# Optimization experiments

Hardware: AMD Instinct MI355X
Metric: run time of the kernel (lower is better)

The kernel has to match this reference:

```python
import jax, jax.numpy as jnp
import numpy as np

NEG_SLOPE = 0.2


def gat_layer(x_src, x_dst, src, dst, W, a_src, a_dst, b, n_dst, H, C):
    # Linear transform: [Ns, H, C] / [Nd, H, C]
    h_s = (x_src @ W).reshape(-1, H, C)
    h_d = (x_dst @ W).reshape(-1, H, C)
    # Per-edge attention logits: a . [x_i || x_j] (x_i = dst/target, x_j = src)
    e = jnp.einsum('ehc,hc->eh', h_s[src], a_src) + jnp.einsum('ehc,hc->eh', h_d[dst], a_dst)
    e = jax.nn.leaky_relu(e, NEG_SLOPE)  # [E, H]
    # Segment softmax over destination neighborhoods
    m = jax.ops.segment_max(e, dst, num_segments=n_dst)          # [Nd, H]
    ex = jnp.exp(e - m[dst])
    denom = jax.ops.segment_sum(ex, dst, num_segments=n_dst)    # [Nd, H]
    alpha = ex / denom[dst]                                      # [E, H]
    # Weighted scatter-sum aggregation
    out = jax.ops.segment_sum(alpha[:, :, None] * h_s[src], dst, num_segments=n_dst)
    return out.reshape(n_dst, H * C) + b


def setup_inputs() -> dict:
    key = jax.random.key(0)
    ks = jax.random.split(key, 16)
    N, F_IN, OUT = 200000, 602, 41
    N1, N1D, E1 = 120000, 30000, 960000
    N2D, E2 = 6000, 192000
    s = 0.05
    return {
        'x': jax.random.normal(ks[0], (N, F_IN), jnp.float32),
        'n_id1': jax.random.randint(ks[1], (N1,), 0, N),
        'res_n_id1': jax.random.randint(ks[2], (N1D,), 0, N1),
        'edge_src1': jax.random.randint(ks[3], (E1,), 0, N1),
        'edge_dst1': jax.random.randint(ks[4], (E1,), 0, N1D),
        'res_n_id2': jax.random.randint(ks[5], (N2D,), 0, N1D),
        'edge_src2': jax.random.randint(ks[6], (E2,), 0, N1D),
        'edge_dst2': jax.random.randint(ks[7], (E2,), 0, N2D),
        'W1': jax.random.normal(ks[8], (F_IN, 64), jnp.float32) * s,
        'att_src1': jax.random.normal(ks[9], (8, 8), jnp.float32) * s,
        'att_dst1': jax.random.normal(ks[10], (8, 8), jnp.float32) * s,
        'bias1': jax.random.normal(ks[11], (64,), jnp.float32) * s,
        'W2': jax.random.normal(ks[12], (64, OUT), jnp.float32) * s,
        'att_src2': jax.random.normal(ks[13], (1, OUT), jnp.float32) * s,
        'att_dst2': jax.random.normal(ks[14], (1, OUT), jnp.float32) * s,
        'bias2': jax.random.normal(ks[15], (OUT,), jnp.float32) * s,
    }


def reference(x, n_id1, res_n_id1, edge_src1, edge_dst1, res_n_id2, edge_src2,
              edge_dst2, W1, att_src1, att_dst1, bias1, W2, att_src2, att_dst2, bias2):
    # Block 1: gather frontier, GATConv(in -> 8, heads=8, concat) -> [N1D, 64]
    h = x[n_id1]
    h = gat_layer(h, h[res_n_id1], edge_src1, edge_dst1,
                  W1, att_src1, att_dst1, bias1, res_n_id1.shape[0], 8, 8)
    h = jax.nn.elu(h)
    # (dropout p=0.6 is identity in eval mode)
    # Block 2: GATConv(64 -> out, heads=1) -> [N2D, out]
    h = gat_layer(h, h[res_n_id2], edge_src2, edge_dst2,
                  W2, att_src2, att_dst2, bias2, res_n_id2.shape[0], 1, W2.shape[1])
    return jax.nn.log_softmax(h, axis=1)
```

## Files before the change

### kernel.cpp

```cpp
#include <hip/hip_runtime.h>
#include <hip/hip_bf16.h>
#include <math.h>

typedef __attribute__((ext_vector_type(8))) short short8;
typedef __attribute__((ext_vector_type(4))) float float4v;

__device__ __forceinline__ float wave_max64(float v) {
#pragma unroll
  for (int o = 32; o > 0; o >>= 1) v = fmaxf(v, __shfl_xor(v, o));
  return v;
}
__device__ __forceinline__ float wave_sum64(float v) {
#pragma unroll
  for (int o = 32; o > 0; o >>= 1) v += __shfl_xor(v, o);
  return v;
}
__device__ __forceinline__ float lrelu02(float v) { return v > 0.f ? v : 0.2f * v; }
__device__ __forceinline__ short bf16_rne(float f) {
  unsigned u = __builtin_bit_cast(unsigned, f);
  unsigned r = (u + 0x7FFFu + ((u >> 16) & 1u)) >> 16;
  return (short)r;
}

__global__ void hist_prepack_kernel(const int* __restrict__ dst1, const int* __restrict__ dst2,
                                    int* __restrict__ counts, const float* __restrict__ W,
                                    short* __restrict__ Wp, int E1, int E2, int N1D, int nbE) {
  int b = blockIdx.x;
  if (b < nbE) {
    int e = b * 256 + threadIdx.x;
    if (e < E1) atomicAdd(&counts[dst1[e]], 1);
    else if (e < E1 + E2) atomicAdd(&counts[N1D + dst2[e - E1]], 1);
  } else {
    int idx = (b - nbE) * 256 + threadIdx.x;
    if (idx >= 19 * 4 * 64) return;
    int lane = idx & 63;
    int t = (idx >> 6) & 3;
    int s = idx >> 8;
    int quad = lane >> 4, n = t * 16 + (lane & 15);
    short8 v;
#pragma unroll
    for (int j = 0; j < 8; j++) {
      int k = s * 32 + quad * 8 + j;
      v[j] = (k < 602) ? bf16_rne(W[k * 64 + n]) : (short)0;
    }
    *((short8*)Wp + idx) = v;
  }
}

__global__ __launch_bounds__(256) void scan1_kernel(const int* __restrict__ counts,
                                                    int* __restrict__ offs,
                                                    int* __restrict__ bsum, int n) {
  __shared__ int ws[4], wpre[4];
  int tid = threadIdx.x, lane = tid & 63, w = tid >> 6;
  int i = blockIdx.x * 256 + tid;
  int v = (i < n) ? counts[i] : 0;
  int x = v;
#pragma unroll
  for (int o = 1; o < 64; o <<= 1) {
    int y = __shfl_up(x, o);
    if (lane >= o) x += y;
  }
  if (lane == 63) ws[w] = x;
  __syncthreads();
  if (tid == 0) {
    int run = 0;
#pragma unroll
    for (int k = 0; k < 4; k++) { wpre[k] = run; run += ws[k]; }
    bsum[blockIdx.x] = run;
  }
  __syncthreads();
  if (i < n) offs[i] = x - v + wpre[w];
}

__global__ __launch_bounds__(256) void scan2_kernel(int* __restrict__ bsum, int nb) {
  __shared__ int ws[4], wpre[4];
  int tid = threadIdx.x, lane = tid & 63, w = tid >> 6;
  int v = (tid < nb) ? bsum[tid] : 0;
  int x = v;
#pragma unroll
  for (int o = 1; o < 64; o <<= 1) {
    int y = __shfl_up(x, o);
    if (lane >= o) x += y;
  }
  if (lane == 63) ws[w] = x;
  __syncthreads();
  if (tid == 0) {
    int run = 0;
#pragma unroll
    for (int k = 0; k < 4; k++) { wpre[k] = run; run += ws[k]; }
  }
  __syncthreads();
  if (tid < nb) bsum[tid] = x - v + wpre[w];
}

__global__ __launch_bounds__(256) void scan3_kernel(int* __restrict__ offs,
                                                    const int* __restrict__ bsum, int n) {
  int i = blockIdx.x * 256 + threadIdx.x;
  if (i < n) offs[i] += bsum[blockIdx.x];
}

__global__ void scatter_kernel(const int* __restrict__ dst1, const int* __restrict__ src1,
                               const int* __restrict__ dst2, const int* __restrict__ src2,
                               int* __restrict__ offs, int* __restrict__ epay,
                               int E1, int E2, int N1D) {
  int e = blockIdx.x * blockDim.x + threadIdx.x;
  if (e < E1) {
    int pos = atomicAdd(&offs[dst1[e]], 1);
    epay[pos] = src1[e];
  } else if (e < E1 + E2) {
    int e2 = e - E1;
    int pos = atomicAdd(&offs[N1D + dst2[e2]], 1);
    epay[pos] = src2[e2];
  }
}

__global__ __launch_bounds__(256) void gemm1_mfma_kernel(const float* __restrict__ x,
                                                         const int* __restrict__ n_id,
                                                         const short* __restrict__ Wp,
                                                         const float* __restrict__ as1,
                                                         float* __restrict__ out,
                                                         float* __restrict__ ssrc, int M) {
  constexpr int K = 602, NSTEP = 19;
  int tid = threadIdx.x;
  int wid = tid >> 6, lane = tid & 63;
  int quad = lane >> 4, mrow = lane & 15;
  int r = blockIdx.x * 64 + wid * 16 + mrow;
  int grow = n_id[r < M ? r : M - 1];
  const float* xrow = x + (size_t)grow * K;
  float4v acc[4] = {{0.f, 0.f, 0.f, 0.f}, {0.f, 0.f, 0.f, 0.f},
                    {0.f, 0.f, 0.f, 0.f}, {0.f, 0.f, 0.f, 0.f}};
  for (int s = 0; s < NSTEP; s++) {
    int k0 = s * 32 + quad * 8;
    float af[8];
    if (k0 + 8 <= K) {
#pragma unroll
      for (int j = 0; j < 8; j += 2) {
        float2 v = *(const float2*)(xrow + k0 + j);
        af[j] = v.x;
        af[j + 1] = v.y;
      }
    } else {
#pragma unroll
      for (int j = 0; j < 8; j++) af[j] = (k0 + j < K) ? xrow[k0 + j] : 0.f;
    }
    short8 a;
#pragma unroll
    for (int j = 0; j < 8; j++) a[j] = bf16_rne(af[j]);
    const short8* wp = (const short8*)Wp + (size_t)s * 256 + lane;
#pragma unroll
    for (int t = 0; t < 4; t++) {
      short8 b = wp[t * 64];
      acc[t] = __builtin_amdgcn_mfma_f32_16x16x32_bf16(a, b, acc[t], 0, 0, 0);
    }
  }
  int rb = blockIdx.x * 64 + wid * 16;
#pragma unroll
  for (int t = 0; t < 4; t++) {
#pragma unroll
    for (int j = 0; j < 4; j++) {
      int rr = rb + quad * 4 + j;
      if (rr < M) out[(size_t)rr * 64 + t * 16 + mrow] = acc[t][j];
    }
  }
  int hi = mrow >> 3, u = mrow & 7;
  float a_s[4];
#pragma unroll
  for (int t = 0; t < 4; t++) a_s[t] = as1[(2 * t + hi) * 8 + u];
#pragma unroll
  for (int t = 0; t < 4; t++) {
#pragma unroll
    for (int j = 0; j < 4; j++) {
      float p = acc[t][j] * a_s[t];
      p += __shfl_xor(p, 1);
      p += __shfl_xor(p, 2);
      p += __shfl_xor(p, 4);
      if (u == j) {
        int rr = rb + quad * 4 + j;
        if (rr < M) ssrc[(size_t)rr * 8 + 2 * t + hi] = p;
      }
    }
  }
}

__global__ __launch_bounds__(256) void agg1_kernel(
    const int* __restrict__ offs, const int* __restrict__ srcs,
    const float* __restrict__ s_src, const int* __restrict__ res,
    const float* __restrict__ ad, const float* __restrict__ hs1,
    const float* __restrict__ bias, const float* __restrict__ W2,
    const float* __restrict__ as2, float* __restrict__ hs2,
    float* __restrict__ ssrc2, int n_dst) {
  constexpr int C = 41;
  __shared__ float Ws[64 * C];
  for (int i = threadIdx.x; i < 64 * C; i += 256) Ws[i] = W2[i];
  __syncthreads();
  int wid = (blockIdx.x * blockDim.x + threadIdx.x) >> 6;
  if (wid >= n_dst) return;
  int lane = threadIdx.x & 63;
  int h = lane >> 3;
  int node = res[wid];
  float v = hs1[(size_t)node * 64 + lane] * ad[lane];
  v += __shfl_xor(v, 1);
  v += __shfl_xor(v, 2);
  v += __shfl_xor(v, 4);
  float sd = v;
  int beg = wid ? offs[wid - 1] : 0;
  int end = offs[wid];
  float mx = -1e30f, den = 0.f, acc = 0.f;
  for (int i = beg; i < end; i += 8) {
    int m = end - i; if (m > 8) m = 8;
    int sr[8]; float ss[8], row[8];
#pragma unroll
    for (int j = 0; j < 8; j++) sr[j] = srcs[i + (j < m ? j : 0)];
#pragma unroll
    for (int j = 0; j < 8; j++) ss[j] = s_src[sr[j] * 8 + h];
#pragma unroll
    for (int j = 0; j < 8; j++) row[j] = hs1[(size_t)sr[j] * 64 + lane];
    float p[8];
#pragma unroll
    for (int j = 0; j < 8; j++) p[j] = (j < m) ? lrelu02(ss[j] + sd) : -1e30f;
    float bm = mx;
#pragma unroll
    for (int j = 0; j < 8; j++) bm = fmaxf(bm, p[j]);
    float scale = __expf(mx - bm);
    den *= scale;
    acc *= scale;
#pragma unroll
    for (int j = 0; j < 8; j++) {
      float w = __expf(p[j] - bm);
      den += w;
      acc += w * row[j];
    }
    mx = bm;
  }
  float val = (end > beg) ? acc / den : 0.f;
  val += bias[lane];
  val = val > 0.f ? val : __expf(val) - 1.f;
  bool act = lane < C;
  int cl = act ? lane : C - 1;
  float acc2 = 0.f;
#pragma unroll
  for (int k = 0; k < 64; k++) {
    float hk = __shfl(val, k);
    acc2 += hk * Ws[k * C + cl];
  }
  float t2 = act ? acc2 * as2[lane] : 0.f;
  float s2 = wave_sum64(t2);
  if (lane == 0) ssrc2[wid] = s2;
  if (act) hs2[(size_t)wid * C + lane] = acc2;
}

__global__ __launch_bounds__(256) void agg2_kernel(
    const int* __restrict__ offs, const int* __restrict__ srcs,
    const float* __restrict__ s_src, const int* __restrict__ res,
    const float* __restrict__ ad, const float* __restrict__ hs2,
    const float* __restrict__ bias, float* __restrict__ out, int n_dst) {
  constexpr int C = 41;
  int wid = (blockIdx.x * blockDim.x + threadIdx.x) >> 6;
  if (wid >= n_dst) return;
  int lane = threadIdx.x & 63;
  bool act = lane < C;
  int node = res[wid];
  float dv = act ? hs2[(size_t)node * C + lane] * ad[lane] : 0.f;
  float sd = wave_sum64(dv);
  int beg = offs[wid - 1];
  int end = offs[wid];
  float mx = -1e30f, den = 0.f, acc = 0.f;
  for (int i = beg; i < end; i += 8) {
    int m = end - i; if (m > 8) m = 8;
    int sr[8]; float ss[8], row[8];
#pragma unroll
    for (int j = 0; j < 8; j++) sr[j] = srcs[i + (j < m ? j : 0)];
#pragma unroll
    for (int j = 0; j < 8; j++) ss[j] = s_src[sr[j]];
#pragma unroll
    for (int j = 0; j < 8; j++) row[j] = act ? hs2[(size_t)sr[j] * C + lane] : 0.f;
    float p[8];
#pragma unroll
    for (int j = 0; j < 8; j++) p[j] = (j < m) ? lrelu02(ss[j] + sd) : -1e30f;
    float bm = mx;
#pragma unroll
    for (int j = 0; j < 8; j++) bm = fmaxf(bm, p[j]);
    float scale = __expf(mx - bm);
    den *= scale;
    acc *= scale;
#pragma unroll
    for (int j = 0; j < 8; j++) {
      float w = __expf(p[j] - bm);
      den += w;
      acc += w * row[j];
    }
    mx = bm;
  }
  float val = (end > beg) ? acc / den : 0.f;
  if (act) val += bias[lane];
  float lv = act ? val : -1e30f;
  float m2 = wave_max64(lv);
  float ex = act ? __expf(val - m2) : 0.f;
  float ssum = wave_sum64(ex);
  if (act) out[(size_t)wid * C + lane] = val - m2 - __logf(ssum);
}

extern "C" void kernel_launch(void* const* d_in, const int* in_sizes, int n_in,
                              void* d_out, int out_size, void* d_ws, size_t ws_size,
                              hipStream_t stream) {
  const float* x    = (const float*)d_in[0];
  const int* n_id1  = (const int*)d_in[1];
  const int* res1   = (const int*)d_in[2];
  const int* esrc1  = (const int*)d_in[3];
  const int* edst1  = (const int*)d_in[4];
  const int* res2   = (const int*)d_in[5];
  const int* esrc2  = (const int*)d_in[6];
  const int* edst2  = (const int*)d_in[7];
  const float* W1   = (const float*)d_in[8];
  const float* as1  = (const float*)d_in[9];
  const float* ad1  = (const float*)d_in[10];
  const float* b1   = (const float*)d_in[11];
  const float* W2   = (const float*)d_in[12];
  const float* as2  = (const float*)d_in[13];
  const float* ad2  = (const float*)d_in[14];
  const float* b2   = (const float*)d_in[15];
  float* out = (float*)d_out;

  const int N1  = in_sizes[1];
  const int N1D = in_sizes[2];
  const int E1  = in_sizes[3];
  const int N2D = in_sizes[5];
  const int E2  = in_sizes[6];
  const int NTOT = N1D + N2D;
  const int ETOT = E1 + E2;

  char* w = (char*)d_ws;
  size_t off = 0;
  auto alloc = [&](size_t bytes) -> void* {
    void* p = (void*)(w + off);
    off += (bytes + 255) & ~(size_t)255;
    return p;
  };
  float* hs1   = (float*)alloc((size_t)N1 * 64 * 4);
  float* ssrc1 = (float*)alloc((size_t)N1 * 8 * 4);
  float* hs2   = (float*)alloc((size_t)N1D * 41 * 4);
  float* ssrc2 = (float*)alloc((size_t)N1D * 4);
  int* counts  = (int*)alloc((size_t)NTOT * 4);
  int* offs    = (int*)alloc((size_t)NTOT * 4);
  int* bsum    = (int*)alloc((size_t)256 * 4);
  int* epay    = (int*)alloc((size_t)ETOT * 4);
  short* Wp    = (short*)alloc((size_t)19 * 4 * 64 * 8 * 2);
  (void)ws_size; (void)n_in; (void)out_size;

  hipMemsetAsync(counts, 0, (size_t)NTOT * 4, stream);

  const int nbE = (ETOT + 255) / 256;
  const int nb = (NTOT + 255) / 256;
  hist_prepack_kernel<<<nbE + 19, 256, 0, stream>>>(edst1, edst2, counts, W1, Wp, E1, E2, N1D, nbE);
  scan1_kernel<<<nb, 256, 0, stream>>>(counts, offs, bsum, NTOT);
  scan2_kernel<<<1, 256, 0, stream>>>(bsum, nb);
  scan3_kernel<<<nb, 256, 0, stream>>>(offs, bsum, NTOT);
  scatter_kernel<<<nbE, 256, 0, stream>>>(edst1, esrc1, edst2, esrc2, offs, epay, E1, E2, N1D);

  gemm1_mfma_kernel<<<(N1 + 63) / 64, 256, 0, stream>>>(x, n_id1, Wp, as1, hs1, ssrc1, N1);
  agg1_kernel<<<(N1D + 3) / 4, 256, 0, stream>>>(offs, epay, ssrc1, res1, ad1, hs1, b1,
                                                 W2, as2, hs2, ssrc2, N1D);

  agg2_kernel<<<(N2D + 3) / 4, 256, 0, stream>>>(offs + N1D, epay, ssrc2, res2, ad2, hs2, b2, out, N2D);
}
```

Baseline: 856.9 us.

## Fuse histogram into GEMM launch, store hs1 as bf16, drop softmax max pass

The edge-count histogram now runs inside the first GEMM kernel, and the memset is replaced by a zeroing pass fused with the weight prepack. The three-kernel scan becomes two, with each block summing the earlier block totals itself. hs1 is stored as bf16 to halve its write and gather traffic, and the online-max rescaling in both aggregation softmaxes is removed. The layer-2 matvec is split into four accumulators for more instruction-level parallelism. Dropping the max subtraction risks exp overflow for large logits, and bf16 storage of hs1 loses precision.

```diff
diff --git a/kernel.cpp b/kernel.cpp
--- a/kernel.cpp
+++ b/kernel.cpp
@@ -11,6 +11,11 @@
   return v;
 }
 __device__ __forceinline__ float wave_sum64(float v) {
+#pragma unroll
+  for (int o = 32; o > 0; o >>= 1) v += __shfl_xor(v, o);
+  return v;
+}
+__device__ __forceinline__ int wave_sum64_i(int v) {
 #pragma unroll
   for (int o = 32; o > 0; o >>= 1) v += __shfl_xor(v, o);
   return v;
@@ -21,17 +26,18 @@
   unsigned r = (u + 0x7FFFu + ((u >> 16) & 1u)) >> 16;
   return (short)r;
 }
-
-__global__ void hist_prepack_kernel(const int* __restrict__ dst1, const int* __restrict__ dst2,
-                                    int* __restrict__ counts, const float* __restrict__ W,
-                                    short* __restrict__ Wp, int E1, int E2, int N1D, int nbE) {
+__device__ __forceinline__ float bf2f(unsigned short u) {
+  return __builtin_bit_cast(float, (unsigned)u << 16);
+}
+
+__global__ void init_prepack_kernel(int* __restrict__ counts, const float* __restrict__ W,
+                                    short* __restrict__ Wp, int ntot, int nbZ) {
   int b = blockIdx.x;
-  if (b < nbE) {
-    int e = b * 256 + threadIdx.x;
-    if (e < E1) atomicAdd(&counts[dst1[e]], 1);
-    else if (e < E1 + E2) atomicAdd(&counts[N1D + dst2[e - E1]], 1);
+  if (b < nbZ) {
+    int i = b * 256 + threadIdx.x;
+    if (i < ntot) counts[i] = 0;
   } else {
-    int idx = (b - nbE) * 256 + threadIdx.x;
+    int idx = (b - nbZ) * 256 + threadIdx.x;
     if (idx >= 19 * 4 * 64) return;
     int lane = idx & 63;
     int t = (idx >> 6) & 3;
@@ -44,6 +50,81 @@
       v[j] = (k < 602) ? bf16_rne(W[k * 64 + n]) : (short)0;
     }
     *((short8*)Wp + idx) = v;
+  }
+}
+
+__global__ __launch_bounds__(256) void hist_gemm1_kernel(
+    const int* __restrict__ dst1, const int* __restrict__ dst2, int* __restrict__ counts,
+    const float* __restrict__ x, const int* __restrict__ n_id, const short* __restrict__ Wp,
+    const float* __restrict__ as1, unsigned short* __restrict__ hs1,
+    float* __restrict__ ssrc, int E1, int E2, int N1D, int nbE, int M) {
+  int b = blockIdx.x;
+  if (b < nbE) {
+    int e = b * 256 + threadIdx.x;
+    if (e < E1) atomicAdd(&counts[dst1[e]], 1);
+    else if (e < E1 + E2) atomicAdd(&counts[N1D + dst2[e - E1]], 1);
+    return;
+  }
+  int gid = b - nbE;
+  constexpr int K = 602, NSTEP = 19;
+  int tid = threadIdx.x;
+  int wid = tid >> 6, lane = tid & 63;
+  int quad = lane >> 4, mrow = lane & 15;
+  int r = gid * 64 + wid * 16 + mrow;
+  int grow = n_id[r < M ? r : M - 1];
+  const float* xrow = x + (size_t)grow * K;
+  float4v acc[4] = {{0.f, 0.f, 0.f, 0.f}, {0.f, 0.f, 0.f, 0.f},
+                    {0.f, 0.f, 0.f, 0.f}, {0.f, 0.f, 0.f, 0.f}};
+  for (int s = 0; s < NSTEP; s++) {
+    int k0 = s * 32 + quad * 8;
+    float af[8];
+    if (k0 + 8 <= K) {
+#pragma unroll
+      for (int j = 0; j < 8; j += 2) {
+        float2 v = *(const float2*)(xrow + k0 + j);
+        af[j] = v.x;
+        af[j + 1] = v.y;
+      }
+    } else {
+#pragma unroll
+      for (int j = 0; j < 8; j++) af[j] = (k0 + j < K) ? xrow[k0 + j] : 0.f;
+    }
+    short8 a;
+#pragma unroll
+    for (int j = 0; j < 8; j++) a[j] = bf16_rne(af[j]);
+    const short8* wp = (const short8*)Wp + (size_t)s * 256 + lane;
+#pragma unroll
+    for (int t = 0; t < 4; t++) {
+      short8 bfr = wp[t * 64];
+      acc[t] = __builtin_amdgcn_mfma_f32_16x16x32_bf16(a, bfr, acc[t], 0, 0, 0);
+    }
+  }
+  int rb = gid * 64 + wid * 16;
+#pragma unroll
+  for (int t = 0; t < 4; t++) {
+#pragma unroll
+    for (int j = 0; j < 4; j++) {
+      int rr = rb + quad * 4 + j;
+      if (rr < M) hs1[(size_t)rr * 64 + t * 16 + mrow] = (unsigned short)bf16_rne(acc[t][j]);
+    }
+  }
+  int hi = mrow >> 3, u = mrow & 7;
+  float a_s[4];
+#pragma unroll
+  for (int t = 0; t < 4; t++) a_s[t] = as1[(2 * t + hi) * 8 + u];
+#pragma unroll
+  for (int t = 0; t < 4; t++) {
+#pragma unroll
+    for (int j = 0; j < 4; j++) {
+      float p = acc[t][j] * a_s[t];
+      p += __shfl_xor(p, 1);
+      p += __shfl_xor(p, 2);
+      p += __shfl_xor(p, 4);
+      if (u == j) {
+        int rr = rb + quad * 4 + j;
+        if (rr < M) ssrc[(size_t)rr * 8 + 2 * t + hi] = p;
+      }
+    }
   }
 }
 
@@ -72,31 +153,18 @@
   if (i < n) offs[i] = x - v + wpre[w];
 }
 
-__global__ __launch_bounds__(256) void scan2_kernel(int* __restrict__ bsum, int nb) {
-  __shared__ int ws[4], wpre[4];
-  int tid = threadIdx.x, lane = tid & 63, w = tid >> 6;
-  int v = (tid < nb) ? bsum[tid] : 0;
-  int x = v;
-#pragma unroll
-  for (int o = 1; o < 64; o <<= 1) {
-    int y = __shfl_up(x, o);
-    if (lane >= o) x += y;
-  }
-  if (lane == 63) ws[w] = x;
+__global__ __launch_bounds__(256) void scan23_kernel(int* __restrict__ offs,
+                                                     const int* __restrict__ bsum, int n) {
+  __shared__ int ws[4];
+  int tid = threadIdx.x;
+  int b = blockIdx.x;
+  int v = (tid < b) ? bsum[tid] : 0;
+  v = wave_sum64_i(v);
+  if ((tid & 63) == 0) ws[tid >> 6] = v;
   __syncthreads();
-  if (tid == 0) {
-    int run = 0;
-#pragma unroll
-    for (int k = 0; k < 4; k++) { wpre[k] = run; run += ws[k]; }
-  }
-  __syncthreads();
-  if (tid < nb) bsum[tid] = x - v + wpre[w];
-}
-
-__global__ __launch_bounds__(256) void scan3_kernel(int* __restrict__ offs,
-                                                    const int* __restrict__ bsum, int n) {
-  int i = blockIdx.x * 256 + threadIdx.x;
-  if (i < n) offs[i] += bsum[blockIdx.x];
+  int pre = ws[0] + ws[1] + ws[2] + ws[3];
+  int i = b * 256 + tid;
+  if (i < n) offs[i] += pre;
 }
 
 __global__ void scatter_kernel(const int* __restrict__ dst1, const int* __restrict__ src1,
@@ -114,78 +182,10 @@
   }
 }
 
-__global__ __launch_bounds__(256) void gemm1_mfma_kernel(const float* __restrict__ x,
-                                                         const int* __restrict__ n_id,
-                                                         const short* __restrict__ Wp,
-                                                         const float* __restrict__ as1,
-                                                         float* __restrict__ out,
-                                                         float* __restrict__ ssrc, int M) {
-  constexpr int K = 602, NSTEP = 19;
-  int tid = threadIdx.x;
-  int wid = tid >> 6, lane = tid & 63;
-  int quad = lane >> 4, mrow = lane & 15;
-  int r = blockIdx.x * 64 + wid * 16 + mrow;
-  int grow = n_id[r < M ? r : M - 1];
-  const float* xrow = x + (size_t)grow * K;
-  float4v acc[4] = {{0.f, 0.f, 0.f, 0.f}, {0.f, 0.f, 0.f, 0.f},
-                    {0.f, 0.f, 0.f, 0.f}, {0.f, 0.f, 0.f, 0.f}};
-  for (int s = 0; s < NSTEP; s++) {
-    int k0 = s * 32 + quad * 8;
-    float af[8];
-    if (k0 + 8 <= K) {
-#pragma unroll
-      for (int j = 0; j < 8; j += 2) {
-        float2 v = *(const float2*)(xrow + k0 + j);
-        af[j] = v.x;
-        af[j + 1] = v.y;
-      }
-    } else {
-#pragma unroll
-      for (int j = 0; j < 8; j++) af[j] = (k0 + j < K) ? xrow[k0 + j] : 0.f;
-    }
-    short8 a;
-#pragma unroll
-    for (int j = 0; j < 8; j++) a[j] = bf16_rne(af[j]);
-    const short8* wp = (const short8*)Wp + (size_t)s * 256 + lane;
-#pragma unroll
-    for (int t = 0; t < 4; t++) {
-      short8 b = wp[t * 64];
-      acc[t] = __builtin_amdgcn_mfma_f32_16x16x32_bf16(a, b, acc[t], 0, 0, 0);
-    }
-  }
-  int rb = blockIdx.x * 64 + wid * 16;
-#pragma unroll
-  for (int t = 0; t < 4; t++) {
-#pragma unroll
-    for (int j = 0; j < 4; j++) {
-      int rr = rb + quad * 4 + j;
-      if (rr < M) out[(size_t)rr * 64 + t * 16 + mrow] = acc[t][j];
-    }
-  }
-  int hi = mrow >> 3, u = mrow & 7;
-  float a_s[4];
-#pragma unroll
-  for (int t = 0; t < 4; t++) a_s[t] = as1[(2 * t + hi) * 8 + u];
-#pragma unroll
-  for (int t = 0; t < 4; t++) {
-#pragma unroll
-    for (int j = 0; j < 4; j++) {
-      float p = acc[t][j] * a_s[t];
-      p += __shfl_xor(p, 1);
-      p += __shfl_xor(p, 2);
-      p += __shfl_xor(p, 4);
-      if (u == j) {
-        int rr = rb + quad * 4 + j;
-        if (rr < M) ssrc[(size_t)rr * 8 + 2 * t + hi] = p;
-      }
-    }
-  }
-}
-
 __global__ __launch_bounds__(256) void agg1_kernel(
     const int* __restrict__ offs, const int* __restrict__ srcs,
     const float* __restrict__ s_src, const int* __restrict__ res,
-    const float* __restrict__ ad, const float* __restrict__ hs1,
+    const float* __restrict__ ad, const unsigned short* __restrict__ hs1,
     const float* __restrict__ bias, const float* __restrict__ W2,
     const float* __restrict__ as2, float* __restrict__ hs2,
     float* __restrict__ ssrc2, int n_dst) {
@@ -198,14 +198,14 @@
   int lane = threadIdx.x & 63;
   int h = lane >> 3;
   int node = res[wid];
-  float v = hs1[(size_t)node * 64 + lane] * ad[lane];
+  float v = bf2f(hs1[(size_t)node * 64 + lane]) * ad[lane];
   v += __shfl_xor(v, 1);
   v += __shfl_xor(v, 2);
   v += __shfl_xor(v, 4);
   float sd = v;
   int beg = wid ? offs[wid - 1] : 0;
   int end = offs[wid];
-  float mx = -1e30f, den = 0.f, acc = 0.f;
+  float den = 0.f, acc = 0.f;
   for (int i = beg; i < end; i += 8) {
     int m = end - i; if (m > 8) m = 8;
     int sr[8]; float ss[8], row[8];
@@ -214,35 +214,30 @@
 #pragma unroll
     for (int j = 0; j < 8; j++) ss[j] = s_src[sr[j] * 8 + h];
 #pragma unroll
-    for (int j = 0; j < 8; j++) row[j] = hs1[(size_t)sr[j] * 64 + lane];
-    float p[8];
-#pragma unroll
-    for (int j = 0; j < 8; j++) p[j] = (j < m) ? lrelu02(ss[j] + sd) : -1e30f;
-    float bm = mx;
-#pragma unroll
-    for (int j = 0; j < 8; j++) bm = fmaxf(bm, p[j]);
-    float scale = __expf(mx - bm);
-    den *= scale;
-    acc *= scale;
+    for (int j = 0; j < 8; j++) row[j] = bf2f(hs1[(size_t)sr[j] * 64 + lane]);
 #pragma unroll
     for (int j = 0; j < 8; j++) {
-      float w = __expf(p[j] - bm);
-      den += w;
-      acc += w * row[j];
-    }
-    mx = bm;
+      if (j < m) {
+        float wgt = __expf(lrelu02(ss[j] + sd));
+        den += wgt;
+        acc += wgt * row[j];
+      }
+    }
   }
   float val = (end > beg) ? acc / den : 0.f;
   val += bias[lane];
   val = val > 0.f ? val : __expf(val) - 1.f;
   bool act = lane < C;
   int cl = act ? lane : C - 1;
-  float acc2 = 0.f;
-#pragma unroll
-  for (int k = 0; k < 64; k++) {
-    float hk = __shfl(val, k);
-    acc2 += hk * Ws[k * C + cl];
-  }
+  float a0 = 0.f, a1 = 0.f, a2 = 0.f, a3 = 0.f;
+#pragma unroll
+  for (int k = 0; k < 64; k += 4) {
+    a0 += __shfl(val, k + 0) * Ws[(k + 0) * C + cl];
+    a1 += __shfl(val, k + 1) * Ws[(k + 1) * C + cl];
+    a2 += __shfl(val, k + 2) * Ws[(k + 2) * C + cl];
+    a3 += __shfl(val, k + 3) * Ws[(k + 3) * C + cl];
+  }
+  float acc2 = (a0 + a1) + (a2 + a3);
   float t2 = act ? acc2 * as2[lane] : 0.f;
   float s2 = wave_sum64(t2);
   if (lane == 0) ssrc2[wid] = s2;
@@ -264,7 +259,7 @@
   float sd = wave_sum64(dv);
   int beg = offs[wid - 1];
   int end = offs[wid];
-  float mx = -1e30f, den = 0.f, acc = 0.f;
+  float den = 0.f, acc = 0.f;
   for (int i = beg; i < end; i += 8) {
     int m = end - i; if (m > 8) m = 8;
     int sr[8]; float ss[8], row[8];
@@ -274,22 +269,14 @@
     for (int j = 0; j < 8; j++) ss[j] = s_src[sr[j]];
 #pragma unroll
     for (int j = 0; j < 8; j++) row[j] = act ? hs2[(size_t)sr[j] * C + lane] : 0.f;
-    float p[8];
-#pragma unroll
-    for (int j = 0; j < 8; j++) p[j] = (j < m) ? lrelu02(ss[j] + sd) : -1e30f;
-    float bm = mx;
-#pragma unroll
-    for (int j = 0; j < 8; j++) bm = fmaxf(bm, p[j]);
-    float scale = __expf(mx - bm);
-    den *= scale;
-    acc *= scale;
 #pragma unroll
     for (int j = 0; j < 8; j++) {
-      float w = __expf(p[j] - bm);
-      den += w;
-      acc += w * row[j];
-    }
-    mx = bm;
+      if (j < m) {
+        float wgt = __expf(lrelu02(ss[j] + sd));
+        den += wgt;
+        acc += wgt * row[j];
+      }
+    }
   }
   float val = (end > beg) ? acc / den : 0.f;
   if (act) val += bias[lane];
@@ -336,7 +323,7 @@
     off += (bytes + 255) & ~(size_t)255;
     return p;
   };
-  float* hs1   = (float*)alloc((size_t)N1 * 64 * 4);
+  unsigned short* hs1 = (unsigned short*)alloc((size_t)N1 * 64 * 2);
   float* ssrc1 = (float*)alloc((size_t)N1 * 8 * 4);
   float* hs2   = (float*)alloc((size_t)N1D * 41 * 4);
   float* ssrc2 = (float*)alloc((size_t)N1D * 4);
@@ -347,19 +334,17 @@
   short* Wp    = (short*)alloc((size_t)19 * 4 * 64 * 8 * 2);
   (void)ws_size; (void)n_in; (void)out_size;
 
-  hipMemsetAsync(counts, 0, (size_t)NTOT * 4, stream);
-
+  const int nbZ = (NTOT + 255) / 256;
   const int nbE = (ETOT + 255) / 256;
-  const int nb = (NTOT + 255) / 256;
-  hist_prepack_kernel<<<nbE + 19, 256, 0, stream>>>(edst1, edst2, counts, W1, Wp, E1, E2, N1D, nbE);
-  scan1_kernel<<<nb, 256, 0, stream>>>(counts, offs, bsum, NTOT);
-  scan2_kernel<<<1, 256, 0, stream>>>(bsum, nb);
-  scan3_kernel<<<nb, 256, 0, stream>>>(offs, bsum, NTOT);
+  const int nbG = (N1 + 63) / 64;
+
+  init_prepack_kernel<<<nbZ + 19, 256, 0, stream>>>(counts, W1, Wp, NTOT, nbZ);
+  hist_gemm1_kernel<<<nbE + nbG, 256, 0, stream>>>(edst1, edst2, counts, x, n_id1, Wp,
+                                                   as1, hs1, ssrc1, E1, E2, N1D, nbE, N1);
+  scan1_kernel<<<nbZ, 256, 0, stream>>>(counts, offs, bsum, NTOT);
+  scan23_kernel<<<nbZ, 256, 0, stream>>>(offs, bsum, NTOT);
   scatter_kernel<<<nbE, 256, 0, stream>>>(edst1, esrc1, edst2, esrc2, offs, epay, E1, E2, N1D);
-
-  gemm1_mfma_kernel<<<(N1 + 63) / 64, 256, 0, stream>>>(x, n_id1, Wp, as1, hs1, ssrc1, N1);
   agg1_kernel<<<(N1D + 3) / 4, 256, 0, stream>>>(offs, epay, ssrc1, res1, ad1, hs1, b1,
                                                  W2, as2, hs2, ssrc2, N1D);
-
   agg2_kernel<<<(N2D + 3) / 4, 256, 0, stream>>>(offs + N1D, epay, ssrc2, res2, ad2, hs2, b2, out, N2D);
 }
```

Measured after the change: 848.3 us. No clear change (-1.0%).
